# Performance work log

Hardware: AMD Instinct MI355X
Metric: run time of the kernel (lower is better)

The kernel has to match this reference:

```python
import jax, jax.numpy as jnp
import numpy as np
from jax import lax

# PRPN constants (match init_kwargs)
NSLOTS = 15
NLOOKBACK = 1
RESOLUTION = 0.1
NLAYERS = 2
H = 1024      # nhid == ninp
NTOKEN = 32000
T, B = 256, 64
INF = 1e8


def masked_softmax(x, mask):
    # PRPN blocks.softmax: exp-normalize then multiply by gate mask
    e = jnp.exp(x - jnp.max(x, axis=-1, keepdims=True))
    e = e * mask
    return e / (jnp.sum(e, axis=-1, keepdims=True) + 1e-8)


def setup_inputs() -> dict:
    key = jax.random.key(0)
    ks = jax.random.split(key, 16)
    s = 0.02
    return {
        'tokens': jax.random.randint(ks[0], (T, B), 0, NTOKEN),
        'emb_table': s * jax.random.normal(ks[1], (NTOKEN, H), jnp.float32),
        'conv1_w': s * jax.random.normal(ks[2], (H, H, NLOOKBACK + 1), jnp.float32),
        'conv1_b': jnp.zeros((H,), jnp.float32),
        'bn1_gamma': jnp.ones((H,), jnp.float32),
        'bn1_beta': jnp.zeros((H,), jnp.float32),
        'conv2_w': s * jax.random.normal(ks[3], (2, H // 2, 1), jnp.float32),
        'conv2_b': jnp.zeros((2,), jnp.float32),
        'reader_wih': s * jax.random.normal(ks[4], (NLAYERS, 4 * H, H), jnp.float32),
        'reader_whh': s * jax.random.normal(ks[5], (NLAYERS, 4 * H, H), jnp.float32),
        'reader_bih': jnp.zeros((NLAYERS, 4 * H), jnp.float32),
        'reader_bhh': jnp.zeros((NLAYERS, 4 * H), jnp.float32),
        'reader_summ_w': s * jax.random.normal(ks[6], (NLAYERS, H, 2 * H), jnp.float32),
        'reader_summ_b': jnp.zeros((NLAYERS, H), jnp.float32),
        'pred_summ_w': s * jax.random.normal(ks[7], (H, 2 * H), jnp.float32),
        'pred_summ_b': jnp.zeros((H,), jnp.float32),
        'ffd_w': s * jax.random.normal(ks[8], (H, 2 * H), jnp.float32),
        'ffd_b': jnp.zeros((H,), jnp.float32),
        'ffd_gamma': jnp.ones((H,), jnp.float32),
        'ffd_beta': jnp.zeros((H,), jnp.float32),
    }


def _parser_gates(emb, conv1_w, conv1_b, bn1_gamma, bn1_beta, conv2_w, conv2_b):
    # emb: (T, B, H). Parser state init: zeros lookback embs, +inf cum_gate.
    t = emb.shape[0]
    emb_last = jnp.concatenate([jnp.zeros((NLOOKBACK,) + emb.shape[1:], emb.dtype), emb], axis=0)
    x = jnp.transpose(emb_last, (1, 2, 0))  # (B, H, T+lookback)
    h = lax.conv_general_dilated(x, conv1_w, (1,), 'VALID',
                                 dimension_numbers=('NCH', 'OIH', 'NCH'))
    h = h + conv1_b[None, :, None]
    h = bn1_gamma[None, :, None] * h + bn1_beta[None, :, None]  # BatchNorm1d (eval, mean=0,var=1)
    h = jax.nn.relu(h)
    g = lax.conv_general_dilated(h, conv2_w, (1,), 'VALID', feature_group_count=2,
                                 dimension_numbers=('NCH', 'OIH', 'NCH'))
    g = jax.nn.sigmoid(g + conv2_b[None, :, None])  # (B, 2, T)
    gate, gate_next = g[:, 0], g[:, 1]  # (B, T)
    cum_gate = jnp.concatenate([jnp.full((gate.shape[0], NSLOTS), INF, gate.dtype), gate], axis=1)
    # gate_hat[:, t, j] = cum_gate[:, (NSLOTS - j) + t], slots stacked for i = NSLOTS..1
    idx = jnp.arange(t)[:, None] + (NSLOTS - jnp.arange(NSLOTS))[None, :]
    gate_hat = cum_gate[:, idx]  # (B, T, NSLOTS)
    mg = jnp.cumprod(jax.nn.sigmoid((gate[:, :, None] - gate_hat) / RESOLUTION * 10 + 5), axis=2)
    mgn = jnp.cumprod(jax.nn.sigmoid((gate_next[:, :, None] - gate_hat) / RESOLUTION * 10 + 5), axis=2)
    return mg, mgn  # (B, T, NSLOTS)


def _prpn_forward(tokens, emb_table, conv1_w, conv1_b, bn1_gamma, bn1_beta, conv2_w, conv2_b,
                  reader_wih, reader_whh, reader_bih, reader_bhh, reader_summ_w, reader_summ_b,
                  pred_summ_w, pred_summ_b, ffd_w, ffd_b, ffd_gamma, ffd_beta):
    t, b = tokens.shape
    emb = emb_table[tokens]  # (T, B, H)
    mg, mgn = _parser_gates(emb, conv1_w, conv1_b, bn1_gamma, bn1_beta, conv2_w, conv2_b)
    mg_t = jnp.transpose(mg, (1, 0, 2))   # (T, B, S)
    mgn_t = jnp.transpose(mgn, (1, 0, 2))
    inv_sqrt_h = 1.0 / np.sqrt(H).astype(np.float32)

    def step(carry, xs):
        rh, rc, pm = carry  # (L,B,S,H), (L,B,S,H), (B,S,H)
        emb_i, mg_i, mgn_i = xs
        h = emb_i
        new_rh, new_rc = [], []
        for j in range(NLAYERS):
            mh, mc = rh[j], rc[j]
            key = jnp.concatenate([h, mh[:, -1]], axis=1) @ reader_summ_w[j].T + reader_summ_b[j]
            logits = jnp.einsum('bsh,bh->bs', mh, key) * inv_sqrt_h
            att = masked_softmax(logits, mg_i)
            sel_h = jnp.einsum('bs,bsh->bh', att, mh)
            sel_c = jnp.einsum('bs,bsh->bh', att, mc)
            gates = h @ reader_wih[j].T + reader_bih[j] + sel_h @ reader_whh[j].T + reader_bhh[j]
            ig, fg, gg, og = jnp.split(gates, 4, axis=1)
            c_new = jax.nn.sigmoid(fg) * sel_c + jax.nn.sigmoid(ig) * jnp.tanh(gg)
            h = jax.nn.sigmoid(og) * jnp.tanh(c_new)
            new_rh.append(jnp.concatenate([mh[:, 1:], h[:, None]], axis=1))
            new_rc.append(jnp.concatenate([mc[:, 1:], c_new[:, None]], axis=1))
        # predictor attention over its own slot memory, gated by memory_gate_next
        key = jnp.concatenate([h, pm[:, -1]], axis=1) @ pred_summ_w.T + pred_summ_b
        logits = jnp.einsum('bsh,bh->bs', pm, key) * inv_sqrt_h
        att = masked_softmax(logits, mgn_i)
        sel = jnp.einsum('bs,bsh->bh', att, pm)
        pm = jnp.concatenate([pm[:, 1:], h[:, None]], axis=1)
        return (jnp.stack(new_rh), jnp.stack(new_rc), pm), (h, sel)

    z = jnp.zeros((NLAYERS, b, NSLOTS, H), emb.dtype)
    carry0 = (z, z, jnp.zeros((b, NSLOTS, H), emb.dtype))
    _, (hs, sels) = lax.scan(step, carry0, (emb, mg_t, mgn_t))
    x = jnp.concatenate([hs.reshape(-1, H), sels.reshape(-1, H)], axis=1)  # (T*B, 2H)
    out = jnp.tanh(ffd_gamma * (x @ ffd_w.T + ffd_b) + ffd_beta)  # PredictNetwork.ffd (BN eval)
    return out


def reference(tokens, emb_table, conv1_w, conv1_b, bn1_gamma, bn1_beta, conv2_w, conv2_b,
              reader_wih, reader_whh, reader_bih, reader_bhh, reader_summ_w, reader_summ_b,
              pred_summ_w, pred_summ_b, ffd_w, ffd_b, ffd_gamma, ffd_beta):
    out = _prpn_forward(tokens, emb_table, conv1_w, conv1_b, bn1_gamma, bn1_beta, conv2_w, conv2_b,
                        reader_wih, reader_whh, reader_bih, reader_bhh, reader_summ_w, reader_summ_b,
                        pred_summ_w, pred_summ_b, ffd_w, ffd_b, ffd_gamma, ffd_beta)
    mask = tokens != 0
    return out, mask
```

## Files before the change

### kernel.cpp

```cpp
#include <hip/hip_runtime.h>


typedef _Float16 half8 __attribute__((ext_vector_type(8)));
typedef float f32x4 __attribute__((ext_vector_type(4)));

#define LSTR 56
#define WSTR 1028
#define ASTR 36

__device__ __forceinline__ float sigm(float x) { return 1.0f / (1.0f + expf(-x)); }

__device__ __forceinline__ void store_ct(float* p, float v)    { *p = v; }
__device__ __forceinline__ void store_ct(_Float16* p, float v) { *p = (_Float16)v; }

__device__ __forceinline__ void mfma_loop(const _Float16* __restrict__ Ag, int lda,
                                          const _Float16* __restrict__ Bg, int ldb,
                                          int K, _Float16* As, _Float16* Bs, f32x4* acc)
{
  const int tid = threadIdx.x;
  const int lr  = tid >> 2;
  const int lc  = (tid & 3) << 3;
  const int ln  = tid & 63;
  const int wv  = tid >> 6;
  const int m15 = ln & 15;
  const int q   = ln >> 4;
  const _Float16* ap = Ag + (size_t)lr * lda + lc;
  const _Float16* bp = Bg + (size_t)lr * ldb + lc;
  _Float16* asw = As + lr * LSTR + lc;
  _Float16* bsw = Bs + lr * LSTR + lc;
  const _Float16* asr = As + (wv * 16 + m15) * LSTR + q * 8;
  const _Float16* bsr = Bs + m15 * LSTR + q * 8;
  half8 av = *(const half8*)ap;
  half8 bv = *(const half8*)bp;
  for (int k0 = 0; k0 < K; k0 += 32) {
    __syncthreads();
    *(half8*)asw = av;
    *(half8*)bsw = bv;
    __syncthreads();
    if (k0 + 32 < K) {
      ap += 32; bp += 32;
      av = *(const half8*)ap;
      bv = *(const half8*)bp;
    }
    half8 a = *(const half8*)asr;
#pragma unroll
    for (int j = 0; j < 4; j++) {
      half8 b = *(const half8*)(bsr + j * 16 * LSTR);
      acc[j] = __builtin_amdgcn_mfma_f32_16x16x32_f16(a, b, acc[j], 0, 0, 0);
    }
  }
}

template <int ACT, typename CT>
__global__ __launch_bounds__(256) void gemm_bt(const _Float16* __restrict__ A, int lda,
                                               const _Float16* __restrict__ B, int ldb,
                                               CT* __restrict__ C, int ldc, int K,
                                               const float* __restrict__ p0,
                                               const float* __restrict__ p1,
                                               const float* __restrict__ p2)
{
  __shared__ __align__(16) _Float16 As[64 * LSTR];
  __shared__ __align__(16) _Float16 Bs[64 * LSTR];
  f32x4 acc[4] = {};
  const int ntile = blockIdx.x, mtile = blockIdx.y;
  mfma_loop(A + (size_t)mtile * 64 * lda, lda, B + (size_t)ntile * 64 * ldb, ldb, K, As, Bs, acc);
  const int ln = threadIdx.x & 63, wv = threadIdx.x >> 6;
  const int m15 = ln & 15, q = ln >> 4;
#pragma unroll
  for (int j = 0; j < 4; j++) {
    const int col = ntile * 64 + j * 16 + m15;
    float b0 = 0.f, b1 = 0.f, b2 = 0.f;
    if (ACT == 0) {
      if (p0) b0 = p0[col];
      if (p1) b0 += p1[col];
    } else {
      b0 = p0[col]; b1 = p1[col]; b2 = p2[col];
    }
#pragma unroll
    for (int r = 0; r < 4; r++) {
      const int row = mtile * 64 + wv * 16 + q * 4 + r;
      float v = acc[j][r];
      if (ACT == 0) v += b0;
      else {
        v = b0 * (v + b1) + b2;
        v = (ACT == 1) ? fmaxf(v, 0.f) : tanhf(v);
      }
      store_ct(&C[(size_t)row * ldc + col], v);
    }
  }
}

__device__ __forceinline__ void mfma_resident(const _Float16* __restrict__ Ag,
                                              const _Float16* __restrict__ W,
                                              _Float16 (*Asd)[64 * ASTR], f32x4* acc)
{
  const int tid = threadIdx.x;
  const int r = tid >> 2, c0 = (tid & 3) << 3;
  const int ln = tid & 63, wv = tid >> 6, m15 = ln & 15, q = ln >> 4;
  const _Float16* ap = Ag + (size_t)r * 1024 + c0;
  half8 av[32];
#pragma unroll
  for (int k = 0; k < 32; ++k) av[k] = *(const half8*)(ap + k * 32);
  const int awoff = r * ASTR + c0;
  const int aroff = (wv * 16 + m15) * ASTR + q * 8;
  const _Float16* wr = W + m15 * WSTR + q * 8;
  *(half8*)(Asd[0] + awoff) = av[0];
#pragma unroll
  for (int k = 0; k < 32; ++k) {
    __syncthreads();
    if (k + 1 < 32) *(half8*)(Asd[(k + 1) & 1] + awoff) = av[k + 1];
    half8 a = *(const half8*)(Asd[k & 1] + aroff);
#pragma unroll
    for (int j = 0; j < 4; j++) {
      half8 b = *(const half8*)(wr + j * 16 * WSTR + k * 32);
      acc[j] = __builtin_amdgcn_mfma_f32_16x16x32_f16(a, b, acc[j], 0, 0, 0);
    }
  }
}

__device__ __forceinline__ void mfma_streamed(const _Float16* __restrict__ Ag,
                                              const _Float16* __restrict__ Bg, int ldb,
                                              _Float16 (*Asd)[64 * ASTR],
                                              _Float16 (*Bsd)[64 * ASTR], f32x4* acc)
{
  const int tid = threadIdx.x;
  const int r = tid >> 2, c0 = (tid & 3) << 3;
  const int ln = tid & 63, wv = tid >> 6, m15 = ln & 15, q = ln >> 4;
  const _Float16* ap = Ag + (size_t)r * 1024 + c0;
  const _Float16* bp = Bg + (size_t)r * ldb + c0;
  half8 av[32], bv[32];
#pragma unroll
  for (int k = 0; k < 16; ++k) {
    av[k] = *(const half8*)(ap + k * 32);
    bv[k] = *(const half8*)(bp + k * 32);
  }
  const int awoff = r * ASTR + c0;
  const int aroff = (wv * 16 + m15) * ASTR + q * 8;
  const int broff = m15 * ASTR + q * 8;
  *(half8*)(Asd[0] + awoff) = av[0];
  *(half8*)(Bsd[0] + awoff) = bv[0];
#pragma unroll
  for (int k = 0; k < 32; ++k) {
    if (k < 16) {
      av[k + 16] = *(const half8*)(ap + (k + 16) * 32);
      bv[k + 16] = *(const half8*)(bp + (k + 16) * 32);
    }
    __syncthreads();
    if (k + 1 < 32) {
      *(half8*)(Asd[(k + 1) & 1] + awoff) = av[k + 1];
      *(half8*)(Bsd[(k + 1) & 1] + awoff) = bv[k + 1];
    }
    half8 a = *(const half8*)(Asd[k & 1] + aroff);
#pragma unroll
    for (int j = 0; j < 4; j++) {
      half8 b = *(const half8*)(Bsd[k & 1] + broff + j * 16 * ASTR);
      acc[j] = __builtin_amdgcn_mfma_f32_16x16x32_f16(a, b, acc[j], 0, 0, 0);
    }
  }
}

__device__ __forceinline__ void store_tile(float* __restrict__ C, int ldc, int nt,
                                           const float* b1, const float* b2, f32x4* acc)
{
  const int ln = threadIdx.x & 63, wv = threadIdx.x >> 6;
  const int m15 = ln & 15, q = ln >> 4;
#pragma unroll
  for (int j = 0; j < 4; j++) {
    const int col = nt * 64 + j * 16 + m15;
    float bb = 0.f;
    if (b1) bb += b1[col];
    if (b2) bb += b2[col];
#pragma unroll
    for (int r = 0; r < 4; r++) {
      const int row = wv * 16 + q * 4 + r;
      C[(size_t)row * ldc + col] = acc[j][r] + bb;
    }
  }
}

template <typename KT, typename GT>
__device__ void cell_body(int b, int c0, int nch, int t,
    const KT* __restrict__ keyA, const float* __restrict__ keyB,
    const GT* __restrict__ gatesIn,
    const float* __restrict__ ringH, const float* __restrict__ ringC,
    const float* __restrict__ proj, const float* __restrict__ mask,
    float* __restrict__ hRingOut, float* __restrict__ cRingOut,
    _Float16* __restrict__ hHalf, float* s_key, float* s_att)
{
  const int tid = threadIdx.x;
  for (int i = tid; i < 1024; i += 256)
    s_key[i] = (float)keyA[b * 1024 + i] + keyB[b * 1024 + i];
  __syncthreads();
  const int wv = tid >> 6, ln = tid & 63;
  for (int s = wv; s < 15; s += 4) {
    const float* hr = ringH + ((size_t)((t + s) & 15) * 64 + b) * 1024;
    float p = 0.f;
    for (int i = ln; i < 1024; i += 64) p = fmaf(hr[i], s_key[i], p);
    for (int off = 32; off > 0; off >>= 1) p += __shfl_down(p, off, 64);
    if (ln == 0) s_att[s] = p * 0.03125f;
  }
  __syncthreads();
  if (tid == 0) {
    float mx = -1e30f;
    for (int s = 0; s < 15; s++) mx = fmaxf(mx, s_att[s]);
    float den = 1e-8f, e[15];
    for (int s = 0; s < 15; s++) { e[s] = expf(s_att[s] - mx) * mask[b * 15 + s]; den += e[s]; }
    float inv = 1.f / den;
    for (int s = 0; s < 15; s++) s_att[s] = e[s] * inv;
  }
  __syncthreads();
  float att[15];
  int poff[15], coff[15];
#pragma unroll
  for (int s = 0; s < 15; s++) {
    att[s] = s_att[s];
    const int phs = (t + s) & 15;
    poff[s] = phs * 262144 + b * 4096;
    coff[s] = phs * 65536 + b * 1024;
  }
  for (int c = c0 + tid; c < c0 + nch; c += 256) {
    float g[4];
#pragma unroll
    for (int gi = 0; gi < 4; gi++) {
      const int gidx = gi * 1024 + c;
      float a = (float)gatesIn[(size_t)b * 4096 + gidx];
      for (int s = 0; s < 15; s++) a = fmaf(att[s], proj[(size_t)poff[s] + gidx], a);
      g[gi] = a;
    }
    float selc = 0.f;
    for (int s = 0; s < 15; s++) selc = fmaf(att[s], ringC[(size_t)coff[s] + c], selc);
    const float ig = sigm(g[0]), fg = sigm(g[1]), gg = tanhf(g[2]), og = sigm(g[3]);
    const float cn = fg * selc + ig * gg;
    const float h  = og * tanhf(cn);
    cRingOut[b * 1024 + c] = cn;
    hRingOut[b * 1024 + c] = h;
    hHalf[b * 1024 + c]    = (_Float16)h;
  }
}

__device__ void pred_body(int b, int c0, int nch, int t,
    const float* __restrict__ keyA, const float* __restrict__ keyB,
    const float* __restrict__ ringH, const float* __restrict__ mask,
    _Float16* __restrict__ xrow, float* s_key, float* s_att)
{
  const int tid = threadIdx.x;
  for (int i = tid; i < 1024; i += 256)
    s_key[i] = keyA[b * 1024 + i] + keyB[b * 1024 + i];
  __syncthreads();
  const int wv = tid >> 6, ln = tid & 63;
  for (int s = wv; s < 15; s += 4) {
    const float* hr = ringH + ((size_t)((t + s) & 15) * 64 + b) * 1024;
    float p = 0.f;
    for (int i = ln; i < 1024; i += 64) p = fmaf(hr[i], s_key[i], p);
    for (int off = 32; off > 0; off >>= 1) p += __shfl_down(p, off, 64);
    if (ln == 0) s_att[s] = p * 0.03125f;
  }
  __syncthreads();
  if (tid == 0) {
    float mx = -1e30f;
    for (int s = 0; s < 15; s++) mx = fmaxf(mx, s_att[s]);
    float den = 1e-8f, e[15];
    for (int s = 0; s < 15; s++) { e[s] = expf(s_att[s] - mx) * mask[b * 15 + s]; den += e[s]; }
    float inv = 1.f / den;
    for (int s = 0; s < 15; s++) s_att[s] = e[s] * inv;
  }
  __syncthreads();
  float att[15];
  int hoff[15];
#pragma unroll
  for (int s = 0; s < 15; s++) { att[s] = s_att[s]; hoff[s] = ((t + s) & 15) * 65536 + b * 1024; }
  const float* hNew = ringH + (size_t)((t + 15) & 15) * 65536 + b * 1024;
  for (int c = c0 + tid; c < c0 + nch; c += 256) {
    float sel = 0.f;
    for (int s = 0; s < 15; s++) sel = fmaf(att[s], ringH[(size_t)hoff[s] + c], sel);
    const float h = hNew[c];
    xrow[(size_t)b * 2048 + c]        = (_Float16)h;
    xrow[(size_t)b * 2048 + 1024 + c] = (_Float16)sel;
  }
}

__device__ __forceinline__ void gsync(unsigned* arrive, unsigned* release, unsigned ph, int bid)
{
  __syncthreads();
  const int tid = threadIdx.x;
  if (bid == 0) {
    if (tid >= 1) {
      while (__hip_atomic_load(&arrive[tid << 5], __ATOMIC_RELAXED, __HIP_MEMORY_SCOPE_AGENT) < ph)
        __builtin_amdgcn_s_sleep(1);
    }
    __syncthreads();
    if (tid == 0) {
      __threadfence();
      __hip_atomic_store(release, ph, __ATOMIC_RELAXED, __HIP_MEMORY_SCOPE_AGENT);
    }
    __syncthreads();
  } else {
    if (tid == 0) {
      __threadfence();
      __hip_atomic_store(&arrive[bid << 5], ph, __ATOMIC_RELAXED, __HIP_MEMORY_SCOPE_AGENT);
      while (__hip_atomic_load(release, __ATOMIC_RELAXED, __HIP_MEMORY_SCOPE_AGENT) < ph)
        __builtin_amdgcn_s_sleep(1);
      __threadfence();
    }
    __syncthreads();
  }
}

struct ScanArgs {
  const _Float16 *embkey, *embgates, *wihF, *whhF, *wsmF, *wpdF;
  const float *mg, *mgn, *bih, *bhh, *bsm, *bpd;
  float *ringH0, *ringC0, *ringH1, *ringC1, *P0, *P1;
  float *kc0, *kc1, *kcp0, *kcp1, *key1s, *gates1i, *keypred;
  _Float16 *h0h, *h1h, *xbuf;
  unsigned *bar;
};

__global__ __launch_bounds__(256, 1) void k_scan(ScanArgs A)
{
  __shared__ __align__(16) _Float16 Wlds[64 * WSTR];
  __shared__ __align__(16) _Float16 Asd[2][64 * ASTR];
  __shared__ __align__(16) _Float16 Bsd[2][64 * ASTR];
  float* s_key = (float*)Bsd;
  float* s_att = (float*)Bsd + 1024;
  const int bid = blockIdx.x;
  unsigned* arrive  = A.bar;
  unsigned* release = A.bar + 8192;
  unsigned ph = 0;

  {
    const _Float16* src; int ldb;
    if (bid < 64)       { src = A.whhF                  + (size_t)bid         * 65536;  ldb = 1024; }
    else if (bid < 80)  { src = A.wsmF + 1024           + (size_t)(bid - 64)  * 131072; ldb = 2048; }
    else if (bid < 144) { src = A.wihF + 4194304        + (size_t)(bid - 80)  * 65536;  ldb = 1024; }
    else if (bid < 160) { src = A.wsmF + 2097152        + (size_t)(bid - 144) * 131072; ldb = 2048; }
    else if (bid < 224) { src = A.whhF + 4194304        + (size_t)(bid - 160) * 65536;  ldb = 1024; }
    else if (bid < 240) { src = A.wsmF + 2097152 + 1024 + (size_t)(bid - 224) * 131072; ldb = 2048; }
    else                { src = A.wpdF                  + (size_t)(bid - 240) * 131072; ldb = 2048; }
    const int r = threadIdx.x >> 2, c0 = (threadIdx.x & 3) << 3;
    for (int it = 0; it < 32; ++it)
      *(half8*)(Wlds + r * WSTR + c0 + it * 32) = *(const half8*)(src + (size_t)r * ldb + c0 + it * 32);
  }

  cell_body<_Float16, _Float16>(bid >> 2, (bid & 3) << 8, 256, 0,
      A.embkey, A.kc0, A.embgates, A.ringH0, A.ringC0, A.P0, A.mg,
      A.ringH0 + (size_t)15 * 65536, A.ringC0 + (size_t)15 * 65536, A.h0h, s_key, s_att);
  gsync(arrive, release, ++ph, bid);

  for (int t = 0; t < 256; ++t) {
    const int w15 = (t + 15) & 15;
    if (bid < 160) {
      float* C; const float* b1 = nullptr; const float* b2 = nullptr; int ldc; int nt;
      if (bid < 64)       { C = A.P0 + (size_t)w15 * 262144; ldc = 4096; nt = bid; }
      else if (bid < 80)  { C = A.kc0;     ldc = 1024; nt = bid - 64; }
      else if (bid < 144) { C = A.gates1i; ldc = 4096; b1 = A.bih + 4096; b2 = A.bhh + 4096; nt = bid - 80; }
      else                { C = A.key1s;   ldc = 1024; b1 = A.bsm + 1024; nt = bid - 144; }
      f32x4 acc[4] = {};
      mfma_resident(A.h0h, Wlds, Asd, acc);
      store_tile(C, ldc, nt, b1, b2, acc);
    } else if (bid < 224 && t > 0) {
      pred_body(bid - 160, 0, 1024, t - 1, A.keypred, ((t - 1) & 1) ? A.kcp0 : A.kcp1,
                A.ringH1, A.mgn + (size_t)(t - 1) * 960, A.xbuf + (size_t)(t - 1) * 131072, s_key, s_att);
    }
    gsync(arrive, release, ++ph, bid);
    cell_body<float, float>(bid >> 2, (bid & 3) << 8, 256, t,
        A.key1s, A.kc1, A.gates1i, A.ringH1, A.ringC1, A.P1, A.mg + (size_t)t * 960,
        A.ringH1 + (size_t)w15 * 65536, A.ringC1 + (size_t)w15 * 65536, A.h1h, s_key, s_att);
    gsync(arrive, release, ++ph, bid);
    if (bid >= 160) {
      float* C; const float* b1 = nullptr; int ldc; int nt;
      if (bid < 224)      { C = A.P1 + (size_t)w15 * 262144; ldc = 4096; nt = bid - 160; }
      else if (bid < 240) { C = A.kc1;     ldc = 1024; nt = bid - 224; }
      else                { C = A.keypred; ldc = 1024; b1 = A.bpd; nt = bid - 240; }
      f32x4 acc[4] = {};
      mfma_resident(A.h1h, Wlds, Asd, acc);
      store_tile(C, ldc, nt, b1, nullptr, acc);
    } else if (bid < 16) {
      float* kcpW = (t & 1) ? A.kcp1 : A.kcp0;
      f32x4 acc[4] = {};
      mfma_streamed(A.h1h, A.wpdF + 1024 + (size_t)bid * 131072, 2048, Asd, Bsd, acc);
      store_tile(kcpW, 1024, bid, nullptr, nullptr, acc);
    } else if (bid < 144 && t < 255) {
      const int bb = (bid - 16) >> 1, c0 = ((bid - 16) & 1) << 9;
      cell_body<_Float16, _Float16>(bb, c0, 512, t + 1,
          A.embkey + (size_t)(t + 1) * 65536, A.kc0, A.embgates + (size_t)(t + 1) * 262144,
          A.ringH0, A.ringC0, A.P0, A.mg + (size_t)(t + 1) * 960,
          A.ringH0 + (size_t)(t & 15) * 65536, A.ringC0 + (size_t)(t & 15) * 65536, A.h0h, s_key, s_att);
    }
    gsync(arrive, release, ++ph, bid);
  }
  pred_body(bid >> 2, (bid & 3) << 8, 256, 255, A.keypred, A.kcp0,
            A.ringH1, A.mgn + (size_t)255 * 960, A.xbuf + (size_t)255 * 131072, s_key, s_att);
}

__global__ void k_zero(float* __restrict__ p, int n) {
  int i = blockIdx.x * 256 + threadIdx.x;
  const int st = gridDim.x * 256;
  for (; i < n; i += st) p[i] = 0.f;
}

__global__ void k_cvt(const float* __restrict__ s, _Float16* __restrict__ d, int n) {
  int i = blockIdx.x * 256 + threadIdx.x;
  const int st = gridDim.x * 256;
  for (; i < n; i += st) d[i] = (_Float16)s[i];
}

__global__ void k_w1r(const float* __restrict__ w, _Float16* __restrict__ d) {
  const int i = blockIdx.x * 256 + threadIdx.x;
  if (i >= 2097152) return;
  const int o = i >> 11, kk = i & 2047;
  const int src = (kk < 1024) ? (o * 2048 + kk * 2) : (o * 2048 + (kk - 1024) * 2 + 1);
  d[i] = (_Float16)w[src];
}

__global__ void k_emb(const int* __restrict__ tokens, const float* __restrict__ table,
                      _Float16* __restrict__ embpair, float* __restrict__ maskOut)
{
  const int tb = blockIdx.x;
  const int t = tb >> 6, b = tb & 63;
  const int tok = tokens[tb];
  const float* row = table + (size_t)tok * 1024;
  _Float16* dst1 = embpair + (size_t)tb * 2048 + 1024;
  for (int i = threadIdx.x; i < 1024; i += 256) {
    const _Float16 v = (_Float16)row[i];
    dst1[i] = v;
    if (t + 1 < 256) embpair[(size_t)(tb + 64) * 2048 + i] = v;
    if (t == 0)      embpair[(size_t)b * 2048 + i] = (_Float16)0.f;
  }
  if (threadIdx.x == 0) maskOut[tb] = (tok != 0) ? 1.f : 0.f;
}

__global__ __launch_bounds__(128) void k_conv2(const _Float16* __restrict__ hcv,
                                               const float* __restrict__ w2, const float* __restrict__ b2,
                                               float* __restrict__ gate, float* __restrict__ gaten)
{
  const int r = blockIdx.x;
  const int wv = threadIdx.x >> 6, ln = threadIdx.x & 63;
  const _Float16* hr = hcv + (size_t)r * 1024 + wv * 512;
  const float* wr = w2 + wv * 512;
  float p = 0.f;
  for (int i = ln; i < 512; i += 64) p = fmaf((float)hr[i], wr[i], p);
  for (int off = 32; off > 0; off >>= 1) p += __shfl_down(p, off, 64);
  if (ln == 0) {
    const float v = sigm(p + b2[wv]);
    (wv ? gaten : gate)[r] = v;
  }
}

__global__ void k_masks(const float* __restrict__ gate, const float* __restrict__ gaten,
                        float* __restrict__ mg, float* __restrict__ mgn)
{
  const int i = blockIdx.x * 256 + threadIdx.x;
  if (i >= 16384) return;
  const int t = i >> 6, b = i & 63;
  const float gc = gate[i], gn = gaten[i];
  float p = 1.f, q = 1.f;
  for (int s = 0; s < 15; s++) {
    const float gh = (s <= t) ? gate[(t - s) * 64 + b] : 1e8f;
    p *= sigm((gc - gh) * 100.f + 5.f);
    q *= sigm((gn - gh) * 100.f + 5.f);
    mg[(size_t)i * 15 + s] = p;
    mgn[(size_t)i * 15 + s] = q;
  }
}

extern "C" void kernel_launch(void* const* d_in, const int* in_sizes, int n_in,
                              void* d_out, int out_size, void* d_ws, size_t ws_size,
                              hipStream_t stream)
{
  (void)in_sizes; (void)n_in; (void)out_size; (void)ws_size;
  const int*   tokens = (const int*)d_in[0];
  const float* table  = (const float*)d_in[1];
  const float* w1     = (const float*)d_in[2];
  const float* c1b    = (const float*)d_in[3];
  const float* g1     = (const float*)d_in[4];
  const float* bt1    = (const float*)d_in[5];
  const float* w2     = (const float*)d_in[6];
  const float* c2b    = (const float*)d_in[7];
  const float* wih    = (const float*)d_in[8];
  const float* whh    = (const float*)d_in[9];
  const float* bih    = (const float*)d_in[10];
  const float* bhh    = (const float*)d_in[11];
  const float* wsm    = (const float*)d_in[12];
  const float* bsm    = (const float*)d_in[13];
  const float* wpd    = (const float*)d_in[14];
  const float* bpd    = (const float*)d_in[15];
  const float* ffw    = (const float*)d_in[16];
  const float* ffb    = (const float*)d_in[17];
  const float* ffg    = (const float*)d_in[18];
  const float* ffbt   = (const float*)d_in[19];

  float* outp    = (float*)d_out;
  float* maskOut = outp + 16777216;

  char* wp_ = (char*)d_ws;
  auto alloc = [&](size_t b) { void* r = (void*)wp_; wp_ += (b + 255) & ~(size_t)255; return r; };

  _Float16* embpair  = (_Float16*)alloc(67108864);
  _Float16* hcv      = (_Float16*)alloc(33554432);
  _Float16* embgates = (_Float16*)alloc(134217728);
  _Float16* wihF     = (_Float16*)alloc(16777216);
  _Float16* whhF     = (_Float16*)alloc(16777216);
  _Float16* wsmF     = (_Float16*)alloc(8388608);
  _Float16* wpdF     = (_Float16*)alloc(4194304);
  _Float16* ffwF     = (_Float16*)alloc(4194304);
  _Float16* w1rF     = (_Float16*)alloc(4194304);
  _Float16* h0h      = (_Float16*)alloc(131072);
  _Float16* h1h      = (_Float16*)alloc(131072);
  float* gate    = (float*)alloc(65536);
  float* gaten   = (float*)alloc(65536);
  float* mg      = (float*)alloc(983040);
  float* mgn     = (float*)alloc(983040);
  float* key1s   = (float*)alloc(262144);
  float* gates1i = (float*)alloc(1048576);
  float* keypred = (float*)alloc(262144);
  float* zb = (float*)alloc(51413120);
  float* ringH0 = zb;
  float* ringC0 = ringH0 + 1048576;
  float* ringH1 = ringC0 + 1048576;
  float* ringC1 = ringH1 + 1048576;
  float* P0     = ringC1 + 1048576;
  float* P1     = P0 + 4194304;
  float* kc0    = P1 + 4194304;
  float* kc1    = kc0 + 65536;
  float* kcp0   = kc1 + 65536;
  float* kcp1   = kcp0 + 65536;
  unsigned* bar = (unsigned*)(kcp1 + 65536);

  _Float16* xbuf   = embpair;
  _Float16* embkey = hcv;

  k_zero<<<4096, 256, 0, stream>>>(zb, 12853280);
  k_emb<<<16384, 256, 0, stream>>>(tokens, table, embpair, maskOut);
  k_cvt<<<8192, 256, 0, stream>>>(wih, wihF, 8388608);
  k_cvt<<<8192, 256, 0, stream>>>(whh, whhF, 8388608);
  k_cvt<<<8192, 256, 0, stream>>>(wsm, wsmF, 4194304);
  k_cvt<<<4096, 256, 0, stream>>>(wpd, wpdF, 2097152);
  k_cvt<<<4096, 256, 0, stream>>>(ffw, ffwF, 2097152);
  k_w1r<<<8192, 256, 0, stream>>>(w1, w1rF);
  gemm_bt<1, _Float16><<<dim3(16, 256), 256, 0, stream>>>(embpair, 2048, w1rF, 2048, hcv, 1024, 2048, g1, c1b, bt1);
  k_conv2<<<16384, 128, 0, stream>>>(hcv, w2, c2b, gate, gaten);
  k_masks<<<64, 256, 0, stream>>>(gate, gaten, mg, mgn);
  gemm_bt<0, _Float16><<<dim3(64, 256), 256, 0, stream>>>(embpair + 1024, 2048, wihF, 1024, embgates, 4096, 1024, bih, bhh, nullptr);
  gemm_bt<0, _Float16><<<dim3(16, 256), 256, 0, stream>>>(embpair + 1024, 2048, wsmF, 2048, embkey, 1024, 1024, bsm, nullptr, nullptr);

  ScanArgs sa;
  sa.embkey = embkey; sa.embgates = embgates;
  sa.wihF = wihF; sa.whhF = whhF; sa.wsmF = wsmF; sa.wpdF = wpdF;
  sa.mg = mg; sa.mgn = mgn; sa.bih = bih; sa.bhh = bhh; sa.bsm = bsm; sa.bpd = bpd;
  sa.ringH0 = ringH0; sa.ringC0 = ringC0; sa.ringH1 = ringH1; sa.ringC1 = ringC1;
  sa.P0 = P0; sa.P1 = P1;
  sa.kc0 = kc0; sa.kc1 = kc1; sa.kcp0 = kcp0; sa.kcp1 = kcp1;
  sa.key1s = key1s; sa.gates1i = gates1i; sa.keypred = keypred;
  sa.h0h = h0h; sa.h1h = h1h; sa.xbuf = xbuf;
  sa.bar = bar;
  k_scan<<<dim3(256), dim3(256), 0, stream>>>(sa);

  gemm_bt<2, float><<<dim3(16, 256), 256, 0, stream>>>(xbuf, 2048, ffwF, 2048, outp, 1024, 2048, ffg, ffb, ffbt);
}
```

Baseline: 30.72 ms.

## Restructure persistent scan into 768 blocks with one barrier per step

Rewrites the persistent scan kernel from 256 blocks with weights resident in LDS and three grid barriers per timestep to 768 blocks (3 per CU) with streamed weights and a single grid barrier per step. Layer-0 cell, layer-1 GEMMs, layer-1 cell and the predictor are pipelined across timesteps in disjoint block groups. The hidden-state rings are stored in fp16 so a separate half copy is not needed, and the streamed GEMM uses a smaller 8-deep register prefetch ring. The intent is to cut grid-synchronisation latency and raise parallelism. In exchange, weights are re-read from global/L2 every step instead of sitting in LDS, and attention dot products now use fp16 h.

New measurement: 33.70 ms. +9.7%, slower.

```diff
diff --git a/kernel.cpp b/kernel.cpp
--- a/kernel.cpp
+++ b/kernel.cpp
@@ -5,7 +5,6 @@
 typedef float f32x4 __attribute__((ext_vector_type(4)));
 
 #define LSTR 56
-#define WSTR 1028
 #define ASTR 36
 
 __device__ __forceinline__ float sigm(float x) { return 1.0f / (1.0f + expf(-x)); }
@@ -90,34 +89,6 @@
   }
 }
 
-__device__ __forceinline__ void mfma_resident(const _Float16* __restrict__ Ag,
-                                              const _Float16* __restrict__ W,
-                                              _Float16 (*Asd)[64 * ASTR], f32x4* acc)
-{
-  const int tid = threadIdx.x;
-  const int r = tid >> 2, c0 = (tid & 3) << 3;
-  const int ln = tid & 63, wv = tid >> 6, m15 = ln & 15, q = ln >> 4;
-  const _Float16* ap = Ag + (size_t)r * 1024 + c0;
-  half8 av[32];
-#pragma unroll
-  for (int k = 0; k < 32; ++k) av[k] = *(const half8*)(ap + k * 32);
-  const int awoff = r * ASTR + c0;
-  const int aroff = (wv * 16 + m15) * ASTR + q * 8;
-  const _Float16* wr = W + m15 * WSTR + q * 8;
-  *(half8*)(Asd[0] + awoff) = av[0];
-#pragma unroll
-  for (int k = 0; k < 32; ++k) {
-    __syncthreads();
-    if (k + 1 < 32) *(half8*)(Asd[(k + 1) & 1] + awoff) = av[k + 1];
-    half8 a = *(const half8*)(Asd[k & 1] + aroff);
-#pragma unroll
-    for (int j = 0; j < 4; j++) {
-      half8 b = *(const half8*)(wr + j * 16 * WSTR + k * 32);
-      acc[j] = __builtin_amdgcn_mfma_f32_16x16x32_f16(a, b, acc[j], 0, 0, 0);
-    }
-  }
-}
-
 __device__ __forceinline__ void mfma_streamed(const _Float16* __restrict__ Ag,
                                               const _Float16* __restrict__ Bg, int ldb,
                                               _Float16 (*Asd)[64 * ASTR],
@@ -128,9 +99,9 @@
   const int ln = tid & 63, wv = tid >> 6, m15 = ln & 15, q = ln >> 4;
   const _Float16* ap = Ag + (size_t)r * 1024 + c0;
   const _Float16* bp = Bg + (size_t)r * ldb + c0;
-  half8 av[32], bv[32];
-#pragma unroll
-  for (int k = 0; k < 16; ++k) {
+  half8 av[8], bv[8];
+#pragma unroll
+  for (int k = 0; k < 8; ++k) {
     av[k] = *(const half8*)(ap + k * 32);
     bv[k] = *(const half8*)(bp + k * 32);
   }
@@ -141,18 +112,18 @@
   *(half8*)(Bsd[0] + awoff) = bv[0];
 #pragma unroll
   for (int k = 0; k < 32; ++k) {
-    if (k < 16) {
-      av[k + 16] = *(const half8*)(ap + (k + 16) * 32);
-      bv[k + 16] = *(const half8*)(bp + (k + 16) * 32);
-    }
     __syncthreads();
     if (k + 1 < 32) {
-      *(half8*)(Asd[(k + 1) & 1] + awoff) = av[k + 1];
-      *(half8*)(Bsd[(k + 1) & 1] + awoff) = bv[k + 1];
+      *(half8*)(Asd[(k + 1) & 1] + awoff) = av[(k + 1) & 7];
+      *(half8*)(Bsd[(k + 1) & 1] + awoff) = bv[(k + 1) & 7];
+      if (k + 9 < 32) {
+        av[(k + 1) & 7] = *(const half8*)(ap + (k + 9) * 32);
+        bv[(k + 1) & 7] = *(const half8*)(bp + (k + 9) * 32);
+      }
     }
     half8 a = *(const half8*)(Asd[k & 1] + aroff);
 #pragma unroll
-    for (int j = 0; j < 4; j++) {
+    for (int j = 0; j < 4; ++j) {
       half8 b = *(const half8*)(Bsd[k & 1] + broff + j * 16 * ASTR);
       acc[j] = __builtin_amdgcn_mfma_f32_16x16x32_f16(a, b, acc[j], 0, 0, 0);
     }
@@ -178,26 +149,40 @@
   }
 }
 
-template <typename KT, typename GT>
-__device__ void cell_body(int b, int c0, int nch, int t,
+template <int NS, typename KT, typename GT>
+__device__ void cell_body(int b, int c0, int ct,
     const KT* __restrict__ keyA, const float* __restrict__ keyB,
     const GT* __restrict__ gatesIn,
-    const float* __restrict__ ringH, const float* __restrict__ ringC,
+    const _Float16* __restrict__ ringHh, const float* __restrict__ ringC,
     const float* __restrict__ proj, const float* __restrict__ mask,
-    float* __restrict__ hRingOut, float* __restrict__ cRingOut,
-    _Float16* __restrict__ hHalf, float* s_key, float* s_att)
+    float* __restrict__ cOut, _Float16* __restrict__ hOut,
+    float* s_key, float* s_att)
 {
   const int tid = threadIdx.x;
-  for (int i = tid; i < 1024; i += 256)
+#pragma unroll
+  for (int k = 0; k < 4; ++k) {
+    const int i = tid + k * 256;
     s_key[i] = (float)keyA[b * 1024 + i] + keyB[b * 1024 + i];
+  }
   __syncthreads();
   const int wv = tid >> 6, ln = tid & 63;
-  for (int s = wv; s < 15; s += 4) {
-    const float* hr = ringH + ((size_t)((t + s) & 15) * 64 + b) * 1024;
-    float p = 0.f;
-    for (int i = ln; i < 1024; i += 64) p = fmaf(hr[i], s_key[i], p);
-    for (int off = 32; off > 0; off >>= 1) p += __shfl_down(p, off, 64);
-    if (ln == 0) s_att[s] = p * 0.03125f;
+#pragma unroll
+  for (int k = 0; k < 4; ++k) {
+    const int s = wv + k * 4;
+    if (s < 15) {
+      const _Float16* hr = ringHh + (size_t)((ct + 2 * NS - 15 + s) % NS) * 65536 + b * 1024;
+      float p = 0.f;
+#pragma unroll
+      for (int rr = 0; rr < 2; ++rr) {
+        const int i = ln * 8 + rr * 512;
+        half8 hv = *(const half8*)(hr + i);
+#pragma unroll
+        for (int e = 0; e < 8; ++e) p = fmaf((float)hv[e], s_key[i + e], p);
+      }
+#pragma unroll
+      for (int off = 32; off > 0; off >>= 1) p += __shfl_down(p, off, 64);
+      if (ln == 0) s_att[s] = p * 0.03125f;
+    }
   }
   __syncthreads();
   if (tid == 0) {
@@ -209,51 +194,64 @@
     for (int s = 0; s < 15; s++) s_att[s] = e[s] * inv;
   }
   __syncthreads();
-  float att[15];
-  int poff[15], coff[15];
+  float att[15]; int poff[15], coff[15];
 #pragma unroll
   for (int s = 0; s < 15; s++) {
     att[s] = s_att[s];
-    const int phs = (t + s) & 15;
-    poff[s] = phs * 262144 + b * 4096;
-    coff[s] = phs * 65536 + b * 1024;
-  }
-  for (int c = c0 + tid; c < c0 + nch; c += 256) {
-    float g[4];
-#pragma unroll
-    for (int gi = 0; gi < 4; gi++) {
-      const int gidx = gi * 1024 + c;
-      float a = (float)gatesIn[(size_t)b * 4096 + gidx];
-      for (int s = 0; s < 15; s++) a = fmaf(att[s], proj[(size_t)poff[s] + gidx], a);
-      g[gi] = a;
-    }
-    float selc = 0.f;
-    for (int s = 0; s < 15; s++) selc = fmaf(att[s], ringC[(size_t)coff[s] + c], selc);
-    const float ig = sigm(g[0]), fg = sigm(g[1]), gg = tanhf(g[2]), og = sigm(g[3]);
-    const float cn = fg * selc + ig * gg;
-    const float h  = og * tanhf(cn);
-    cRingOut[b * 1024 + c] = cn;
-    hRingOut[b * 1024 + c] = h;
-    hHalf[b * 1024 + c]    = (_Float16)h;
-  }
-}
-
-__device__ void pred_body(int b, int c0, int nch, int t,
+    const int sl = (ct + 17 + s) & 15;
+    poff[s] = sl * 262144 + b * 4096;
+    coff[s] = sl * 65536 + b * 1024;
+  }
+  const int c = c0 + tid;
+  float g[4];
+#pragma unroll
+  for (int gi = 0; gi < 4; gi++) {
+    const int gidx = gi * 1024 + c;
+    float a = (float)gatesIn[(size_t)b * 4096 + gidx];
+#pragma unroll
+    for (int s = 0; s < 15; s++) a = fmaf(att[s], proj[(size_t)poff[s] + gidx], a);
+    g[gi] = a;
+  }
+  float selc = 0.f;
+#pragma unroll
+  for (int s = 0; s < 15; s++) selc = fmaf(att[s], ringC[(size_t)coff[s] + c], selc);
+  const float ig = sigm(g[0]), fg = sigm(g[1]), gg = tanhf(g[2]), og = sigm(g[3]);
+  const float cn = fg * selc + ig * gg;
+  const float h  = og * tanhf(cn);
+  cOut[b * 1024 + c] = cn;
+  hOut[b * 1024 + c] = (_Float16)h;
+}
+
+__device__ void pred_body(int b, int c0, int pt,
     const float* __restrict__ keyA, const float* __restrict__ keyB,
-    const float* __restrict__ ringH, const float* __restrict__ mask,
+    const _Float16* __restrict__ ringHh, const float* __restrict__ mask,
     _Float16* __restrict__ xrow, float* s_key, float* s_att)
 {
   const int tid = threadIdx.x;
-  for (int i = tid; i < 1024; i += 256)
+#pragma unroll
+  for (int k = 0; k < 4; ++k) {
+    const int i = tid + k * 256;
     s_key[i] = keyA[b * 1024 + i] + keyB[b * 1024 + i];
+  }
   __syncthreads();
   const int wv = tid >> 6, ln = tid & 63;
-  for (int s = wv; s < 15; s += 4) {
-    const float* hr = ringH + ((size_t)((t + s) & 15) * 64 + b) * 1024;
-    float p = 0.f;
-    for (int i = ln; i < 1024; i += 64) p = fmaf(hr[i], s_key[i], p);
-    for (int off = 32; off > 0; off >>= 1) p += __shfl_down(p, off, 64);
-    if (ln == 0) s_att[s] = p * 0.03125f;
+#pragma unroll
+  for (int k = 0; k < 4; ++k) {
+    const int s = wv + k * 4;
+    if (s < 15) {
+      const _Float16* hr = ringHh + (size_t)((pt + 19 + s) % 17) * 65536 + b * 1024;
+      float p = 0.f;
+#pragma unroll
+      for (int rr = 0; rr < 2; ++rr) {
+        const int i = ln * 8 + rr * 512;
+        half8 hv = *(const half8*)(hr + i);
+#pragma unroll
+        for (int e = 0; e < 8; ++e) p = fmaf((float)hv[e], s_key[i + e], p);
+      }
+#pragma unroll
+      for (int off = 32; off > 0; off >>= 1) p += __shfl_down(p, off, 64);
+      if (ln == 0) s_att[s] = p * 0.03125f;
+    }
   }
   __syncthreads();
   if (tid == 0) {
@@ -265,18 +263,19 @@
     for (int s = 0; s < 15; s++) s_att[s] = e[s] * inv;
   }
   __syncthreads();
-  float att[15];
-  int hoff[15];
-#pragma unroll
-  for (int s = 0; s < 15; s++) { att[s] = s_att[s]; hoff[s] = ((t + s) & 15) * 65536 + b * 1024; }
-  const float* hNew = ringH + (size_t)((t + 15) & 15) * 65536 + b * 1024;
-  for (int c = c0 + tid; c < c0 + nch; c += 256) {
-    float sel = 0.f;
-    for (int s = 0; s < 15; s++) sel = fmaf(att[s], ringH[(size_t)hoff[s] + c], sel);
-    const float h = hNew[c];
-    xrow[(size_t)b * 2048 + c]        = (_Float16)h;
-    xrow[(size_t)b * 2048 + 1024 + c] = (_Float16)sel;
-  }
+  float att[15]; int hoff[15];
+#pragma unroll
+  for (int s = 0; s < 15; s++) {
+    att[s] = s_att[s];
+    hoff[s] = ((pt + 19 + s) % 17) * 65536 + b * 1024;
+  }
+  const _Float16* hNew = ringHh + (size_t)((pt + 17) % 17) * 65536 + b * 1024;
+  const int c = c0 + tid;
+  float sel = 0.f;
+#pragma unroll
+  for (int s = 0; s < 15; s++) sel = fmaf(att[s], (float)ringHh[(size_t)hoff[s] + c], sel);
+  xrow[(size_t)b * 2048 + c]        = hNew[c];
+  xrow[(size_t)b * 2048 + 1024 + c] = (_Float16)sel;
 }
 
 __device__ __forceinline__ void gsync(unsigned* arrive, unsigned* release, unsigned ph, int bid)
@@ -284,9 +283,13 @@
   __syncthreads();
   const int tid = threadIdx.x;
   if (bid == 0) {
-    if (tid >= 1) {
-      while (__hip_atomic_load(&arrive[tid << 5], __ATOMIC_RELAXED, __HIP_MEMORY_SCOPE_AGENT) < ph)
-        __builtin_amdgcn_s_sleep(1);
+#pragma unroll
+    for (int k = 0; k < 3; ++k) {
+      const int idx = tid + k * 256;
+      if (idx > 0) {
+        while (__hip_atomic_load(&arrive[idx << 5], __ATOMIC_RELAXED, __HIP_MEMORY_SCOPE_AGENT) < ph)
+          __builtin_amdgcn_s_sleep(1);
+      }
     }
     __syncthreads();
     if (tid == 0) {
@@ -309,87 +312,80 @@
 struct ScanArgs {
   const _Float16 *embkey, *embgates, *wihF, *whhF, *wsmF, *wpdF;
   const float *mg, *mgn, *bih, *bhh, *bsm, *bpd;
-  float *ringH0, *ringC0, *ringH1, *ringC1, *P0, *P1;
+  _Float16 *ringH0h, *ringH1h;
+  float *ringC0, *ringC1, *P0, *P1;
   float *kc0, *kc1, *kcp0, *kcp1, *key1s, *gates1i, *keypred;
-  _Float16 *h0h, *h1h, *xbuf;
+  _Float16 *xbuf;
   unsigned *bar;
 };
 
-__global__ __launch_bounds__(256, 1) void k_scan(ScanArgs A)
-{
-  __shared__ __align__(16) _Float16 Wlds[64 * WSTR];
+__global__ __launch_bounds__(256, 3) void k_scan(ScanArgs A)
+{
   __shared__ __align__(16) _Float16 Asd[2][64 * ASTR];
   __shared__ __align__(16) _Float16 Bsd[2][64 * ASTR];
-  float* s_key = (float*)Bsd;
-  float* s_att = (float*)Bsd + 1024;
+  float* s_key = (float*)Asd;
+  float* s_att = (float*)Bsd;
   const int bid = blockIdx.x;
   unsigned* arrive  = A.bar;
-  unsigned* release = A.bar + 8192;
+  unsigned* release = A.bar + 768 * 32;
   unsigned ph = 0;
 
-  {
-    const _Float16* src; int ldb;
-    if (bid < 64)       { src = A.whhF                  + (size_t)bid         * 65536;  ldb = 1024; }
-    else if (bid < 80)  { src = A.wsmF + 1024           + (size_t)(bid - 64)  * 131072; ldb = 2048; }
-    else if (bid < 144) { src = A.wihF + 4194304        + (size_t)(bid - 80)  * 65536;  ldb = 1024; }
-    else if (bid < 160) { src = A.wsmF + 2097152        + (size_t)(bid - 144) * 131072; ldb = 2048; }
-    else if (bid < 224) { src = A.whhF + 4194304        + (size_t)(bid - 160) * 65536;  ldb = 1024; }
-    else if (bid < 240) { src = A.wsmF + 2097152 + 1024 + (size_t)(bid - 224) * 131072; ldb = 2048; }
-    else                { src = A.wpdF                  + (size_t)(bid - 240) * 131072; ldb = 2048; }
-    const int r = threadIdx.x >> 2, c0 = (threadIdx.x & 3) << 3;
-    for (int it = 0; it < 32; ++it)
-      *(half8*)(Wlds + r * WSTR + c0 + it * 32) = *(const half8*)(src + (size_t)r * ldb + c0 + it * 32);
-  }
-
-  cell_body<_Float16, _Float16>(bid >> 2, (bid & 3) << 8, 256, 0,
-      A.embkey, A.kc0, A.embgates, A.ringH0, A.ringC0, A.P0, A.mg,
-      A.ringH0 + (size_t)15 * 65536, A.ringC0 + (size_t)15 * 65536, A.h0h, s_key, s_att);
+  if (bid >= 256 && bid < 512) {
+    const int q = bid - 256;
+    cell_body<16, _Float16, _Float16>(q >> 2, (q & 3) << 8, 0,
+        A.embkey, A.kc0, A.embgates, A.ringH0h, A.ringC0, A.P0, A.mg,
+        A.ringC0, A.ringH0h, s_key, s_att);
+  }
   gsync(arrive, release, ++ph, bid);
 
-  for (int t = 0; t < 256; ++t) {
-    const int w15 = (t + 15) & 15;
+  for (int t = 0; t <= 256; ++t) {
     if (bid < 160) {
-      float* C; const float* b1 = nullptr; const float* b2 = nullptr; int ldc; int nt;
-      if (bid < 64)       { C = A.P0 + (size_t)w15 * 262144; ldc = 4096; nt = bid; }
-      else if (bid < 80)  { C = A.kc0;     ldc = 1024; nt = bid - 64; }
-      else if (bid < 144) { C = A.gates1i; ldc = 4096; b1 = A.bih + 4096; b2 = A.bhh + 4096; nt = bid - 80; }
-      else                { C = A.key1s;   ldc = 1024; b1 = A.bsm + 1024; nt = bid - 144; }
+      if (t < 256) {
+        const _Float16* B; float* C; const float* b1 = nullptr; const float* b2 = nullptr;
+        int ldb, ldc, nt;
+        if (bid < 64)       { B = A.whhF;             C = A.P0 + (size_t)(t & 15) * 262144; ldb = 1024; ldc = 4096; nt = bid; }
+        else if (bid < 80)  { B = A.wsmF + 1024;      C = A.kc0;     ldb = 2048; ldc = 1024; nt = bid - 64; }
+        else if (bid < 144) { B = A.wihF + 4194304;   C = A.gates1i; b1 = A.bih + 4096; b2 = A.bhh + 4096; ldb = 1024; ldc = 4096; nt = bid - 80; }
+        else                { B = A.wsmF + 2097152;   C = A.key1s;   b1 = A.bsm + 1024; ldb = 2048; ldc = 1024; nt = bid - 144; }
+        f32x4 acc[4] = {};
+        mfma_streamed(A.ringH0h + (size_t)(t & 15) * 65536, B + (size_t)nt * 64 * ldb, ldb, Asd, Bsd, acc);
+        store_tile(C, ldc, nt, b1, b2, acc);
+      }
+    } else if (bid < 272 && t > 0) {
+      const int u = bid - 160;
+      const _Float16* B; float* C; const float* b1 = nullptr; int ldb, ldc, nt;
+      if (u < 64)       { B = A.whhF + 4194304;        C = A.P1 + (size_t)((t - 1) & 15) * 262144; ldb = 1024; ldc = 4096; nt = u; }
+      else if (u < 80)  { B = A.wsmF + 2097152 + 1024; C = A.kc1;     ldb = 2048; ldc = 1024; nt = u - 64; }
+      else if (u < 96)  { B = A.wpdF;                  C = A.keypred; b1 = A.bpd; ldb = 2048; ldc = 1024; nt = u - 80; }
+      else              { B = A.wpdF + 1024;           C = ((t - 1) & 1) ? A.kcp1 : A.kcp0; ldb = 2048; ldc = 1024; nt = u - 96; }
       f32x4 acc[4] = {};
-      mfma_resident(A.h0h, Wlds, Asd, acc);
-      store_tile(C, ldc, nt, b1, b2, acc);
-    } else if (bid < 224 && t > 0) {
-      pred_body(bid - 160, 0, 1024, t - 1, A.keypred, ((t - 1) & 1) ? A.kcp0 : A.kcp1,
-                A.ringH1, A.mgn + (size_t)(t - 1) * 960, A.xbuf + (size_t)(t - 1) * 131072, s_key, s_att);
+      mfma_streamed(A.ringH1h + (size_t)((t + 16) % 17) * 65536, B + (size_t)nt * 64 * ldb, ldb, Asd, Bsd, acc);
+      store_tile(C, ldc, nt, b1, nullptr, acc);
     }
     gsync(arrive, release, ++ph, bid);
-    cell_body<float, float>(bid >> 2, (bid & 3) << 8, 256, t,
-        A.key1s, A.kc1, A.gates1i, A.ringH1, A.ringC1, A.P1, A.mg + (size_t)t * 960,
-        A.ringH1 + (size_t)w15 * 65536, A.ringC1 + (size_t)w15 * 65536, A.h1h, s_key, s_att);
-    gsync(arrive, release, ++ph, bid);
-    if (bid >= 160) {
-      float* C; const float* b1 = nullptr; int ldc; int nt;
-      if (bid < 224)      { C = A.P1 + (size_t)w15 * 262144; ldc = 4096; nt = bid - 160; }
-      else if (bid < 240) { C = A.kc1;     ldc = 1024; nt = bid - 224; }
-      else                { C = A.keypred; ldc = 1024; b1 = A.bpd; nt = bid - 240; }
-      f32x4 acc[4] = {};
-      mfma_resident(A.h1h, Wlds, Asd, acc);
-      store_tile(C, ldc, nt, b1, nullptr, acc);
-    } else if (bid < 16) {
-      float* kcpW = (t & 1) ? A.kcp1 : A.kcp0;
-      f32x4 acc[4] = {};
-      mfma_streamed(A.h1h, A.wpdF + 1024 + (size_t)bid * 131072, 2048, Asd, Bsd, acc);
-      store_tile(kcpW, 1024, bid, nullptr, nullptr, acc);
-    } else if (bid < 144 && t < 255) {
-      const int bb = (bid - 16) >> 1, c0 = ((bid - 16) & 1) << 9;
-      cell_body<_Float16, _Float16>(bb, c0, 512, t + 1,
-          A.embkey + (size_t)(t + 1) * 65536, A.kc0, A.embgates + (size_t)(t + 1) * 262144,
-          A.ringH0, A.ringC0, A.P0, A.mg + (size_t)(t + 1) * 960,
-          A.ringH0 + (size_t)(t & 15) * 65536, A.ringC0 + (size_t)(t & 15) * 65536, A.h0h, s_key, s_att);
-    }
-    gsync(arrive, release, ++ph, bid);
-  }
-  pred_body(bid >> 2, (bid & 3) << 8, 256, 255, A.keypred, A.kcp0,
-            A.ringH1, A.mgn + (size_t)255 * 960, A.xbuf + (size_t)255 * 131072, s_key, s_att);
+
+    if (bid < 256) {
+      if (t < 256)
+        cell_body<17, float, float>(bid >> 2, (bid & 3) << 8, t,
+            A.key1s, A.kc1, A.gates1i, A.ringH1h, A.ringC1, A.P1, A.mg + (size_t)t * 960,
+            A.ringC1 + (size_t)(t & 15) * 65536, A.ringH1h + (size_t)(t % 17) * 65536, s_key, s_att);
+    } else if (bid < 512) {
+      if (t < 255) {
+        const int q = bid - 256;
+        cell_body<16, _Float16, _Float16>(q >> 2, (q & 3) << 8, t + 1,
+            A.embkey + (size_t)(t + 1) * 65536, A.kc0, A.embgates + (size_t)(t + 1) * 262144,
+            A.ringH0h, A.ringC0, A.P0, A.mg + (size_t)(t + 1) * 960,
+            A.ringC0 + (size_t)((t + 1) & 15) * 65536, A.ringH0h + (size_t)((t + 1) & 15) * 65536,
+            s_key, s_att);
+      }
+    } else if (bid < 768 && t > 0) {
+      const int q = bid - 512;
+      pred_body(q >> 2, (q & 3) << 8, t - 1,
+          A.keypred, (t & 1) ? A.kcp1 : A.kcp0,
+          A.ringH1h, A.mgn + (size_t)(t - 1) * 960, A.xbuf + (size_t)(t - 1) * 131072, s_key, s_att);
+    }
+    if (t < 256) gsync(arrive, release, ++ph, bid);
+  }
 }
 
 __global__ void k_zero(float* __restrict__ p, int n) {
@@ -504,8 +500,6 @@
   _Float16* wpdF     = (_Float16*)alloc(4194304);
   _Float16* ffwF     = (_Float16*)alloc(4194304);
   _Float16* w1rF     = (_Float16*)alloc(4194304);
-  _Float16* h0h      = (_Float16*)alloc(131072);
-  _Float16* h1h      = (_Float16*)alloc(131072);
   float* gate    = (float*)alloc(65536);
   float* gaten   = (float*)alloc(65536);
   float* mg      = (float*)alloc(983040);
@@ -513,23 +507,23 @@
   float* key1s   = (float*)alloc(262144);
   float* gates1i = (float*)alloc(1048576);
   float* keypred = (float*)alloc(262144);
-  float* zb = (float*)alloc(51413120);
-  float* ringH0 = zb;
-  float* ringC0 = ringH0 + 1048576;
-  float* ringH1 = ringC0 + 1048576;
-  float* ringC1 = ringH1 + 1048576;
-  float* P0     = ringC1 + 1048576;
-  float* P1     = P0 + 4194304;
-  float* kc0    = P1 + 4194304;
-  float* kc1    = kc0 + 65536;
-  float* kcp0   = kc1 + 65536;
-  float* kcp1   = kcp0 + 65536;
-  unsigned* bar = (unsigned*)(kcp1 + 65536);
+  char* zbc = (char*)alloc(47415424);
+  float*    P0      = (float*)zbc;
+  float*    P1      = (float*)(zbc + 16777216);
+  float*    ringC0  = (float*)(zbc + 33554432);
+  float*    ringC1  = (float*)(zbc + 37748736);
+  _Float16* ringH0h = (_Float16*)(zbc + 41943040);
+  _Float16* ringH1h = (_Float16*)(zbc + 44040192);
+  float*    kc0     = (float*)(zbc + 46268416);
+  float*    kc1     = (float*)(zbc + 46530560);
+  float*    kcp0    = (float*)(zbc + 46792704);
+  float*    kcp1    = (float*)(zbc + 47054848);
+  unsigned* bar     = (unsigned*)(zbc + 47316992);
 
   _Float16* xbuf   = embpair;
   _Float16* embkey = hcv;
 
-  k_zero<<<4096, 256, 0, stream>>>(zb, 12853280);
+  k_zero<<<4096, 256, 0, stream>>>((float*)zbc, 11853856);
   k_emb<<<16384, 256, 0, stream>>>(tokens, table, embpair, maskOut);
   k_cvt<<<8192, 256, 0, stream>>>(wih, wihF, 8388608);
   k_cvt<<<8192, 256, 0, stream>>>(whh, whhF, 8388608);
@@ -547,13 +541,12 @@
   sa.embkey = embkey; sa.embgates = embgates;
   sa.wihF = wihF; sa.whhF = whhF; sa.wsmF = wsmF; sa.wpdF = wpdF;
   sa.mg = mg; sa.mgn = mgn; sa.bih = bih; sa.bhh = bhh; sa.bsm = bsm; sa.bpd = bpd;
-  sa.ringH0 = ringH0; sa.ringC0 = ringC0; sa.ringH1 = ringH1; sa.ringC1 = ringC1;
-  sa.P0 = P0; sa.P1 = P1;
+  sa.ringH0h = ringH0h; sa.ringH1h = ringH1h;
+  sa.ringC0 = ringC0; sa.ringC1 = ringC1; sa.P0 = P0; sa.P1 = P1;
   sa.kc0 = kc0; sa.kc1 = kc1; sa.kcp0 = kcp0; sa.kcp1 = kcp1;
   sa.key1s = key1s; sa.gates1i = gates1i; sa.keypred = keypred;
-  sa.h0h = h0h; sa.h1h = h1h; sa.xbuf = xbuf;
-  sa.bar = bar;
-  k_scan<<<dim3(256), dim3(256), 0, stream>>>(sa);
+  sa.xbuf = xbuf; sa.bar = bar;
+  k_scan<<<dim3(768), dim3(256), 0, stream>>>(sa);
 
   gemm_bt<2, float><<<dim3(16, 256), 256, 0, stream>>>(xbuf, 2048, ffwF, 2048, outp, 1024, 2048, ffg, ffb, ffbt);
 }
```
